# Kernel optimization log

Hardware: AMD Instinct MI355X
Metric: run time of the kernel (lower is better)

The kernel has to match this reference:

```python
import jax, jax.numpy as jnp
import numpy as np

WINDOW = 5
MAX_LEVELS = 4
EPS = 1e-6

_SX = (jnp.array([[-1., 0., 1.], [-2., 0., 2.], [-1., 0., 1.]], dtype=jnp.float32) / 8.0).reshape(1, 1, 3, 3)
_SY = jnp.transpose(_SX, (0, 1, 3, 2))
_DN = ('NCHW', 'OIHW', 'NCHW')


def _avg_pool2(x):
    B, C, H, W = x.shape
    return x.reshape(B, C, H // 2, 2, W // 2, 2).mean(axis=(3, 5))


def _warp(img, flow):
    # bilinear grid_sample, align_corners=True, zeros padding; sample at pixel coords grid+flow
    B, C, H, W = img.shape
    ys, xs = jnp.meshgrid(jnp.arange(H, dtype=img.dtype), jnp.arange(W, dtype=img.dtype), indexing='ij')
    x = xs[None] + flow[:, 0]  # [B,H,W]
    y = ys[None] + flow[:, 1]
    x0f, y0f = jnp.floor(x), jnp.floor(y)
    wx, wy = x - x0f, y - y0f
    imf = img.reshape(B, C, H * W)

    def gather(yi, xi):
        valid = (xi >= 0) & (xi <= W - 1) & (yi >= 0) & (yi <= H - 1)
        xi_c = jnp.clip(xi, 0, W - 1).astype(jnp.int32)
        yi_c = jnp.clip(yi, 0, H - 1).astype(jnp.int32)
        flat = (yi_c * W + xi_c).reshape(B, 1, H * W)
        v = jnp.take_along_axis(imf, jnp.broadcast_to(flat, (B, C, H * W)), axis=2).reshape(B, C, H, W)
        return v * valid[:, None].astype(img.dtype)

    out = (gather(y0f, x0f) * ((1 - wx) * (1 - wy))[:, None]
           + gather(y0f, x0f + 1) * (wx * (1 - wy))[:, None]
           + gather(y0f + 1, x0f) * ((1 - wx) * wy)[:, None]
           + gather(y0f + 1, x0f + 1) * (wx * wy)[:, None])
    return out


def _resize_ac(x, Hn, Wn):
    # bilinear resize, align_corners=True (static shapes)
    B, C, H, W = x.shape
    if (H, W) == (Hn, Wn):
        return x
    ys = jnp.linspace(0.0, H - 1, Hn, dtype=x.dtype)
    xs = jnp.linspace(0.0, W - 1, Wn, dtype=x.dtype)
    y0 = jnp.clip(jnp.floor(ys), 0, H - 2).astype(jnp.int32)
    x0 = jnp.clip(jnp.floor(xs), 0, W - 2).astype(jnp.int32)
    wy = (ys - y0)[None, None, :, None]
    wx = (xs - x0)[None, None, None, :]
    rows = x[:, :, y0, :] * (1 - wy) + x[:, :, y0 + 1, :] * wy
    return rows[:, :, :, x0] * (1 - wx) + rows[:, :, :, x0 + 1] * wx


def _lucas_kanade(I1, I2):
    if I1.shape[1] > 1:
        I1 = I1.mean(1, keepdims=True)
        I2 = I2.mean(1, keepdims=True)
    Ix = jax.lax.conv_general_dilated(I1, _SX, (1, 1), [(1, 1), (1, 1)], dimension_numbers=_DN)
    Iy = jax.lax.conv_general_dilated(I1, _SY, (1, 1), [(1, 1), (1, 1)], dimension_numbers=_DN)
    It = I2 - I1
    # stack all 5 structure-tensor products and box-filter them with one grouped conv
    stats = jnp.concatenate([Ix * Ix, Iy * Iy, Ix * Iy, Ix * It, Iy * It], axis=1)  # [B,5,H,W]
    boxk = jnp.ones((5, 1, WINDOW, WINDOW), dtype=I1.dtype)
    p0 = WINDOW // 2
    p1 = WINDOW - p0 - 1
    S = jax.lax.conv_general_dilated(stats, boxk, (1, 1), [(p0, p1), (p0, p1)],
                                     feature_group_count=5, dimension_numbers=_DN)
    Sxx, Syy, Sxy, Sxt, Syt = jnp.split(S, 5, axis=1)
    inv = 1.0 / (Sxx * Syy - Sxy * Sxy + EPS)
    u = (-Syy * Sxt + Sxy * Syt) * inv
    v = (Sxy * Sxt - Sxx * Syt) * inv
    return jnp.concatenate([u, v], axis=1)


def setup_inputs() -> dict:
    key = jax.random.key(0)
    k1, k2 = jax.random.split(key)
    img1 = jax.random.uniform(k1, (8, 3, 512, 512), dtype=jnp.float32)
    img2 = jax.random.uniform(k2, (8, 3, 512, 512), dtype=jnp.float32)
    return {"img1": img1, "img2": img2}


def reference(img1, img2):
    B, C, H, W = img1.shape
    levels = max(1, MAX_LEVELS)
    pyr1, pyr2 = [img1], [img2]
    for _ in range(1, levels):
        pyr1.append(_avg_pool2(pyr1[-1]))
        pyr2.append(_avg_pool2(pyr2[-1]))
    flow = jnp.zeros((B, 2, pyr1[-1].shape[2], pyr1[-1].shape[3]), dtype=img1.dtype)
    for lvl in range(levels - 1, -1, -1):
        I1, I2 = pyr1[lvl], pyr2[lvl]
        if lvl < levels - 1:
            flow = _resize_ac(flow, I1.shape[2], I1.shape[3]) * 2.0
        I2w = _warp(I2, flow)
        flow = flow + _lucas_kanade(I1, I2w)
    if flow.shape[2:] != (H, W):
        fh, fw = flow.shape[2], flow.shape[3]
        flow = _resize_ac(flow, H, W)
        flow = flow * jnp.array([W / fw, H / fh], dtype=flow.dtype).reshape(1, 2, 1, 1)
    return flow
```

## Files before the change

### kernel.cpp

```cpp
#include <hip/hip_runtime.h>

#define NB 8

typedef float f2 __attribute__((ext_vector_type(2)));


__device__ __forceinline__ void gray_item(
    int i, const float* __restrict__ img1, const float* __restrict__ img2,
    float* __restrict__ g0a, float* __restrict__ g0b,
    float* __restrict__ g1a, float* __restrict__ g1b) {
    const int W = 512, HW = 512 * 512, Wq = 256, HWq = 256 * 256;
    int qx = i % Wq;
    int qy = (i / Wq) % Wq;
    int b = i / HWq;
    size_t base = (size_t)b * 3 * HW + (size_t)(2 * qy) * W + 2 * qx;
    const float third = 1.0f / 3.0f;

    f2 a0c0 = __builtin_nontemporal_load((const f2*)(img1 + base));
    f2 a1c0 = __builtin_nontemporal_load((const f2*)(img1 + base + W));
    f2 a0c1 = __builtin_nontemporal_load((const f2*)(img1 + base + HW));
    f2 a1c1 = __builtin_nontemporal_load((const f2*)(img1 + base + HW + W));
    f2 a0c2 = __builtin_nontemporal_load((const f2*)(img1 + base + 2 * HW));
    f2 a1c2 = __builtin_nontemporal_load((const f2*)(img1 + base + 2 * HW + W));
    float p00 = (a0c0.x + a0c1.x + a0c2.x) * third;
    float p01 = (a0c0.y + a0c1.y + a0c2.y) * third;
    float p10 = (a1c0.x + a1c1.x + a1c2.x) * third;
    float p11 = (a1c0.y + a1c1.y + a1c2.y) * third;
    size_t gbase = (size_t)b * HW + (size_t)(2 * qy) * W + 2 * qx;
    *(f2*)(g0a + gbase) = (f2){p00, p01};
    *(f2*)(g0a + gbase + W) = (f2){p10, p11};
    g1a[(size_t)b * HWq + qy * Wq + qx] = (p00 + p01 + p10 + p11) * 0.25f;

    f2 b0c0 = __builtin_nontemporal_load((const f2*)(img2 + base));
    f2 b1c0 = __builtin_nontemporal_load((const f2*)(img2 + base + W));
    f2 b0c1 = __builtin_nontemporal_load((const f2*)(img2 + base + HW));
    f2 b1c1 = __builtin_nontemporal_load((const f2*)(img2 + base + HW + W));
    f2 b0c2 = __builtin_nontemporal_load((const f2*)(img2 + base + 2 * HW));
    f2 b1c2 = __builtin_nontemporal_load((const f2*)(img2 + base + 2 * HW + W));
    float q00 = (b0c0.x + b0c1.x + b0c2.x) * third;
    float q01 = (b0c0.y + b0c1.y + b0c2.y) * third;
    float q10 = (b1c0.x + b1c1.x + b1c2.x) * third;
    float q11 = (b1c0.y + b1c1.y + b1c2.y) * third;
    *(f2*)(g0b + gbase) = (f2){q00, q01};
    *(f2*)(g0b + gbase + W) = (f2){q10, q11};
    g1b[(size_t)b * HWq + qy * Wq + qx] = (q00 + q01 + q10 + q11) * 0.25f;
}

__device__ __forceinline__ void down2_item(
    int i, const float* __restrict__ l1a, const float* __restrict__ l1b,
    float* __restrict__ l2a, float* __restrict__ l2b,
    float* __restrict__ l3a, float* __restrict__ l3b) {
    const int W3 = 64, W2 = 128, W1 = 256;
    int x3 = i % W3;
    int y3 = (i / W3) % W3;
    int b = (i / (W3 * W3)) % NB;
    int j = i / (NB * W3 * W3);
    const float* l1 = (j ? l1b : l1a) + (size_t)b * W1 * W1;
    float* l2 = (j ? l2b : l2a) + (size_t)b * W2 * W2;
    float* l3 = (j ? l3b : l3a) + (size_t)b * W3 * W3;
    float4 r0 = *(const float4*)(l1 + (size_t)(4 * y3 + 0) * W1 + 4 * x3);
    float4 r1 = *(const float4*)(l1 + (size_t)(4 * y3 + 1) * W1 + 4 * x3);
    float4 r2 = *(const float4*)(l1 + (size_t)(4 * y3 + 2) * W1 + 4 * x3);
    float4 r3 = *(const float4*)(l1 + (size_t)(4 * y3 + 3) * W1 + 4 * x3);
    float a00 = (r0.x + r0.y + r1.x + r1.y) * 0.25f;
    float a01 = (r0.z + r0.w + r1.z + r1.w) * 0.25f;
    float a10 = (r2.x + r2.y + r3.x + r3.y) * 0.25f;
    float a11 = (r2.z + r2.w + r3.z + r3.w) * 0.25f;
    *(f2*)(l2 + (size_t)(2 * y3) * W2 + 2 * x3) = (f2){a00, a01};
    *(f2*)(l2 + (size_t)(2 * y3 + 1) * W2 + 2 * x3) = (f2){a10, a11};
    l3[y3 * W3 + x3] = (a00 + a01 + a10 + a11) * 0.25f;
}

template <int MODE, int H, int W, int TH>
__device__ __forceinline__ void lk_strip(
    int b, int tix, const float* __restrict__ g1, const float* __restrict__ g2,
    const float* __restrict__ fin, float* __restrict__ fout) {
    constexpr int XT = (W + 57) / 58;
    constexpr int NR = TH + 4;
    constexpr int Hs = H / 2, Ws = W / 2;
    constexpr float scale = (float)(Hs - 1) / (float)(H - 1);

    const int lane = threadIdx.x & 63;
    const int xt = tix % XT, yt = tix / XT;
    const int x = xt * 58 - 3 + lane;
    const bool xin = (x >= 0) && (x < W);

    const float* G1 = g1 + (size_t)b * H * W;
    const float* G2 = g2 + (size_t)b * H * W;
    float* FO = fout + (size_t)b * 2 * H * W;

    const int p0 = yt * TH - 2;

    auto issue1 = [&](int yy) -> float {
        return (xin && yy >= 0 && yy < H) ? G1[yy * W + x] : 0.0f;
    };
    auto dands = [&](float gv, float& d, float& s) {
        float gl = __shfl_up(gv, 1);
        float gr = __shfl_down(gv, 1);
        d = gr - gl;
        s = gl + 2.0f * gv + gr;
    };
    auto hs5 = [&](float v) {
        float a = __shfl_down(v, 1);
        float c = __shfl_down(v, 2);
        float t = v + a + c;
        return __shfl_up(t, 2) + a + c;
    };

    float g[NR + 2];
#pragma unroll
    for (int j = 0; j < NR + 2; ++j) g[j] = issue1(p0 - 1 + j);

    float i2d[MODE ? 1 : NR];
    if (!MODE) {
#pragma unroll
        for (int i = 0; i < NR; ++i) {
            int yc = p0 + i;
            i2d[i] = (xin && yc >= 0 && yc < H) ? G2[yc * W + x] : 0.0f;
        }
    }

    float su[MODE ? NR : 1], sv[MODE ? NR : 1];
    float w00[MODE ? NR : 1], w01[MODE ? NR : 1], w10[MODE ? NR : 1], w11[MODE ? NR : 1];
    if (MODE) {
        const float* FU = fin + (size_t)b * 2 * Hs * Ws;
        const float* FV = FU + Hs * Ws;
        float sx = (float)x * scale;
        int cx0 = min(max((int)sx, 0), Ws - 2);
        float wxf = sx - (float)cx0;
        int y0cur = min(max((int)((float)p0 * scale), 0), Hs - 2);
        const float* pu = FU + y0cur * Ws + cx0;
        const float* pv = FV + y0cur * Ws + cx0;
        float u00 = pu[0], u01 = pu[1], u10 = pu[Ws], u11 = pu[Ws + 1];
        float v00 = pv[0], v01 = pv[1], v10 = pv[Ws], v11 = pv[Ws + 1];
#pragma unroll
        for (int i = 0; i < NR; ++i) {
            int yc = p0 + i;
            int y0i = min(max((int)((float)yc * scale), 0), Hs - 2);
            if (y0i != y0cur) {
                u00 = u10; u01 = u11; v00 = v10; v01 = v11;
                const float* qu = FU + (y0i + 1) * Ws + cx0;
                const float* qv = FV + (y0i + 1) * Ws + cx0;
                u10 = qu[0]; u11 = qu[1];
                v10 = qv[0]; v11 = qv[1];
                y0cur = y0i;
            }
            float wyf = (float)yc * scale - (float)y0cur;
            float ut = u00 + (u10 - u00) * wyf;
            float ub = u01 + (u11 - u01) * wyf;
            float vt = v00 + (v10 - v00) * wyf;
            float vb = v01 + (v11 - v01) * wyf;
            su[i] = 2.0f * (ut + (ub - ut) * wxf);
            sv[i] = 2.0f * (vt + (vb - vt) * wxf);
            float xx = (float)x + su[i], yy2 = (float)yc + sv[i];
            int xi = (int)floorf(xx), yi = (int)floorf(yy2);
            int xa = min(max(xi, 0), W - 1), xb = min(max(xi + 1, 0), W - 1);
            int ya = min(max(yi, 0), H - 1), yb = min(max(yi + 1, 0), H - 1);
            w00[i] = G2[ya * W + xa];
            w01[i] = G2[ya * W + xb];
            w10[i] = G2[yb * W + xa];
            w11[i] = G2[yb * W + xb];
        }
    }

    float hxx[5], hyy[5], hxy[5], hxt[5], hyt[5];
#pragma unroll
    for (int k = 0; k < 5; ++k) { hxx[k] = hyy[k] = hxy[k] = hxt[k] = hyt[k] = 0.0f; }

    float dm, d0, sm, s0, dp, sp;
    dands(g[0], dm, sm);
    dands(g[1], d0, s0);

#pragma unroll
    for (int i = 0; i < NR; ++i) {
        const int yc = p0 + i;
        dands(g[i + 2], dp, sp);
        float Ix = (dm + 2.0f * d0 + dp) * 0.125f;
        float Iy = (sp - sm) * 0.125f;

        float I2w;
        if (MODE) {
            float xx = (float)x + su[i], yy2 = (float)yc + sv[i];
            float x0f = floorf(xx), y0f = floorf(yy2);
            float wx = xx - x0f, wy = yy2 - y0f;
            int xi = (int)x0f, yi = (int)y0f;
            float mx0 = (xi >= 0 && xi < W) ? 1.0f : 0.0f;
            float mx1 = (xi >= -1 && xi < W - 1) ? 1.0f : 0.0f;
            float my0 = (yi >= 0 && yi < H) ? 1.0f : 0.0f;
            float my1 = (yi >= -1 && yi < H - 1) ? 1.0f : 0.0f;
            I2w = w00[i] * ((1.0f - wx) * (1.0f - wy) * mx0 * my0)
                + w01[i] * (wx * (1.0f - wy) * mx1 * my0)
                + w10[i] * ((1.0f - wx) * wy * mx0 * my1)
                + w11[i] * (wx * wy * mx1 * my1);
        } else {
            I2w = i2d[i];
        }
        float It = I2w - g[i + 1];
        float vm = (xin && yc >= 0 && yc < H) ? 1.0f : 0.0f;
        Ix *= vm; Iy *= vm; It *= vm;

        const int k = i % 5;
        hxx[k] = Ix * Ix;
        hyy[k] = Iy * Iy;
        hxy[k] = Ix * Iy;
        hxt[k] = Ix * It;
        hyt[k] = Iy * It;

        if (i >= 4) {
            float vxx = hxx[0] + hxx[1] + hxx[2] + hxx[3] + hxx[4];
            float vyy = hyy[0] + hyy[1] + hyy[2] + hyy[3] + hyy[4];
            float vxy = hxy[0] + hxy[1] + hxy[2] + hxy[3] + hxy[4];
            float vxt = hxt[0] + hxt[1] + hxt[2] + hxt[3] + hxt[4];
            float vyt = hyt[0] + hyt[1] + hyt[2] + hyt[3] + hyt[4];
            float Sxx = hs5(vxx);
            float Syy = hs5(vyy);
            float Sxy = hs5(vxy);
            float Sxt = hs5(vxt);
            float Syt = hs5(vyt);
            float inv = 1.0f / (Sxx * Syy - Sxy * Sxy + 1e-6f);
            float du = (-Syy * Sxt + Sxy * Syt) * inv;
            float dv = (Sxy * Sxt - Sxx * Syt) * inv;
            int yo = yc - 2;
            if (lane >= 3 && lane <= 60 && x < W) {
                float ou = du, ov = dv;
                if (MODE) { ou += su[i - 2]; ov += sv[i - 2]; }
                FO[yo * W + x] = ou;
                FO[H * W + yo * W + x] = ov;
            }
        }
        dm = d0; d0 = dp;
        sm = s0; s0 = sp;
    }
}


__global__ void gray_pool_kernel(const float* __restrict__ img1, const float* __restrict__ img2,
                                 float* __restrict__ g0a, float* __restrict__ g0b,
                                 float* __restrict__ g1a, float* __restrict__ g1b) {
    int i = blockIdx.x * blockDim.x + threadIdx.x;
    if (i >= NB * 256 * 256) return;
    gray_item(i, img1, img2, g0a, g0b, g1a, g1b);
}

__global__ void down2_kernel(const float* __restrict__ l1a, const float* __restrict__ l1b,
                             float* __restrict__ l2a, float* __restrict__ l2b,
                             float* __restrict__ l3a, float* __restrict__ l3b) {
    int i = blockIdx.x * blockDim.x + threadIdx.x;
    if (i >= 2 * NB * 64 * 64) return;
    down2_item(i, l1a, l1b, l2a, l2b, l3a, l3b);
}

template <int MODE, int H, int W, int TH>
__global__ __launch_bounds__(256, 4) void lk_roll(
    const float* __restrict__ g1, const float* __restrict__ g2,
    const float* __restrict__ fin, float* __restrict__ fout) {
    constexpr int XT = (W + 57) / 58;
    constexpr int TILES = XT * (H / TH);
    const int wid = threadIdx.x >> 6;
    const int b = blockIdx.x % NB;
    const int tix = (blockIdx.x / NB) * 4 + wid;
    if (tix >= TILES) return;
    lk_strip<MODE, H, W, TH>(b, tix, g1, g2, fin, fout);
}

extern "C" void kernel_launch(void* const* d_in, const int* in_sizes, int n_in,
                              void* d_out, int out_size, void* d_ws, size_t ws_size,
                              hipStream_t stream) {
    const float* img1 = (const float*)d_in[0];
    const float* img2 = (const float*)d_in[1];
    float* out = (float*)d_out;
    float* ws = (float*)d_ws;

    constexpr size_t HW0 = 512 * 512, HW1 = 256 * 256, HW2 = 128 * 128, HW3 = 64 * 64;
    constexpr size_t TOT = NB * (HW0 + HW1 + HW2 + HW3);
    float* p1 = ws;
    float* p2 = ws + TOT;
    float* f64 = p2 + TOT;
    float* f128 = f64 + NB * 2 * HW3;
    float* f256 = f128 + NB * 2 * HW2;
    float* p1_0 = p1, * p1_1 = p1 + NB * HW0, * p1_2 = p1_1 + NB * HW1, * p1_3 = p1_2 + NB * HW2;
    float* p2_0 = p2, * p2_1 = p2 + NB * HW0, * p2_2 = p2_1 + NB * HW1, * p2_3 = p2_2 + NB * HW2;

    {
        int n = NB * 256 * 256;
        gray_pool_kernel<<<(n + 255) / 256, 256, 0, stream>>>(img1, img2, p1_0, p2_0, p1_1, p2_1);
    }
    {
        int n = 2 * NB * 64 * 64;
        down2_kernel<<<(n + 255) / 256, 256, 0, stream>>>(p1_1, p2_1, p1_2, p2_2, p1_3, p2_3);
    }
    {
        constexpr int tiles = 2 * 64;
        lk_roll<0, 64, 64, 1><<<NB * ((tiles + 3) / 4), 256, 0, stream>>>(p1_3, p2_3, nullptr, f64);
    }
    {
        constexpr int tiles = 3 * 128;
        lk_roll<1, 128, 128, 1><<<NB * ((tiles + 3) / 4), 256, 0, stream>>>(p1_2, p2_2, f64, f128);
    }
    {
        constexpr int tiles = 5 * 128;
        lk_roll<1, 256, 256, 2><<<NB * ((tiles + 3) / 4), 256, 0, stream>>>(p1_1, p2_1, f128, f256);
    }
    {
        constexpr int tiles = 9 * 128;
        lk_roll<1, 512, 512, 4><<<NB * ((tiles + 3) / 4), 256, 0, stream>>>(p1_0, p2_0, f256, out);
    }
}
```

Before: 64.14 us.

## Fuse grayscale and full pyramid construction into one tiled kernel

Replaces the separate gray/pool and down2 kernels with a single kernel. Each block handles a 16x16 tile of level 1 and builds levels 2 and 3 from shared memory, which removes one launch and the global re-read of level 1. It adds two block barriers with mostly idle threads in the later stages, and block-to-tile mapping changes coalescing (16-wide rows). Separately, the flow upsampling loop now reloads four neighbours per row instead of carrying rows over, which simplifies control flow at the cost of extra cached loads.

```diff
diff --git a/kernel.cpp b/kernel.cpp
--- a/kernel.cpp
+++ b/kernel.cpp
@@ -4,16 +4,24 @@
 
 typedef float f2 __attribute__((ext_vector_type(2)));
 
-
-__device__ __forceinline__ void gray_item(
-    int i, const float* __restrict__ img1, const float* __restrict__ img2,
+__global__ __launch_bounds__(256) void gray_pyr_kernel(
+    const float* __restrict__ img1, const float* __restrict__ img2,
     float* __restrict__ g0a, float* __restrict__ g0b,
-    float* __restrict__ g1a, float* __restrict__ g1b) {
-    const int W = 512, HW = 512 * 512, Wq = 256, HWq = 256 * 256;
-    int qx = i % Wq;
-    int qy = (i / Wq) % Wq;
-    int b = i / HWq;
-    size_t base = (size_t)b * 3 * HW + (size_t)(2 * qy) * W + 2 * qx;
+    float* __restrict__ g1a, float* __restrict__ g1b,
+    float* __restrict__ g2a, float* __restrict__ g2b,
+    float* __restrict__ g3a, float* __restrict__ g3b) {
+    const int W = 512, HW = 512 * 512;
+    __shared__ float sL1a[16][17], sL1b[16][17];
+    __shared__ float sL2a[8][9], sL2b[8][9];
+
+    int blk = blockIdx.x;
+    int b = blk % NB;
+    int t = blk / NB;
+    int ty = t / 16, tx = t % 16;
+    int lx = threadIdx.x % 16, ly = threadIdx.x / 16;
+    int y1 = ty * 16 + ly, x1 = tx * 16 + lx;
+
+    size_t base = (size_t)b * 3 * HW + (size_t)(2 * y1) * W + 2 * x1;
     const float third = 1.0f / 3.0f;
 
     f2 a0c0 = __builtin_nontemporal_load((const f2*)(img1 + base));
@@ -26,10 +34,12 @@
     float p01 = (a0c0.y + a0c1.y + a0c2.y) * third;
     float p10 = (a1c0.x + a1c1.x + a1c2.x) * third;
     float p11 = (a1c0.y + a1c1.y + a1c2.y) * third;
-    size_t gbase = (size_t)b * HW + (size_t)(2 * qy) * W + 2 * qx;
+    size_t gbase = (size_t)b * HW + (size_t)(2 * y1) * W + 2 * x1;
     *(f2*)(g0a + gbase) = (f2){p00, p01};
     *(f2*)(g0a + gbase + W) = (f2){p10, p11};
-    g1a[(size_t)b * HWq + qy * Wq + qx] = (p00 + p01 + p10 + p11) * 0.25f;
+    float pa = (p00 + p01 + p10 + p11) * 0.25f;
+    g1a[(size_t)b * 256 * 256 + y1 * 256 + x1] = pa;
+    sL1a[ly][lx] = pa;
 
     f2 b0c0 = __builtin_nontemporal_load((const f2*)(img2 + base));
     f2 b1c0 = __builtin_nontemporal_load((const f2*)(img2 + base + W));
@@ -43,32 +53,33 @@
     float q11 = (b1c0.y + b1c1.y + b1c2.y) * third;
     *(f2*)(g0b + gbase) = (f2){q00, q01};
     *(f2*)(g0b + gbase + W) = (f2){q10, q11};
-    g1b[(size_t)b * HWq + qy * Wq + qx] = (q00 + q01 + q10 + q11) * 0.25f;
-}
-
-__device__ __forceinline__ void down2_item(
-    int i, const float* __restrict__ l1a, const float* __restrict__ l1b,
-    float* __restrict__ l2a, float* __restrict__ l2b,
-    float* __restrict__ l3a, float* __restrict__ l3b) {
-    const int W3 = 64, W2 = 128, W1 = 256;
-    int x3 = i % W3;
-    int y3 = (i / W3) % W3;
-    int b = (i / (W3 * W3)) % NB;
-    int j = i / (NB * W3 * W3);
-    const float* l1 = (j ? l1b : l1a) + (size_t)b * W1 * W1;
-    float* l2 = (j ? l2b : l2a) + (size_t)b * W2 * W2;
-    float* l3 = (j ? l3b : l3a) + (size_t)b * W3 * W3;
-    float4 r0 = *(const float4*)(l1 + (size_t)(4 * y3 + 0) * W1 + 4 * x3);
-    float4 r1 = *(const float4*)(l1 + (size_t)(4 * y3 + 1) * W1 + 4 * x3);
-    float4 r2 = *(const float4*)(l1 + (size_t)(4 * y3 + 2) * W1 + 4 * x3);
-    float4 r3 = *(const float4*)(l1 + (size_t)(4 * y3 + 3) * W1 + 4 * x3);
-    float a00 = (r0.x + r0.y + r1.x + r1.y) * 0.25f;
-    float a01 = (r0.z + r0.w + r1.z + r1.w) * 0.25f;
-    float a10 = (r2.x + r2.y + r3.x + r3.y) * 0.25f;
-    float a11 = (r2.z + r2.w + r3.z + r3.w) * 0.25f;
-    *(f2*)(l2 + (size_t)(2 * y3) * W2 + 2 * x3) = (f2){a00, a01};
-    *(f2*)(l2 + (size_t)(2 * y3 + 1) * W2 + 2 * x3) = (f2){a10, a11};
-    l3[y3 * W3 + x3] = (a00 + a01 + a10 + a11) * 0.25f;
+    float pb = (q00 + q01 + q10 + q11) * 0.25f;
+    g1b[(size_t)b * 256 * 256 + y1 * 256 + x1] = pb;
+    sL1b[ly][lx] = pb;
+    __syncthreads();
+
+    if (threadIdx.x < 64) {
+        int y2 = threadIdx.x / 8, x2 = threadIdx.x % 8;
+        float va = (sL1a[2 * y2][2 * x2] + sL1a[2 * y2][2 * x2 + 1]
+                  + sL1a[2 * y2 + 1][2 * x2] + sL1a[2 * y2 + 1][2 * x2 + 1]) * 0.25f;
+        float vb = (sL1b[2 * y2][2 * x2] + sL1b[2 * y2][2 * x2 + 1]
+                  + sL1b[2 * y2 + 1][2 * x2] + sL1b[2 * y2 + 1][2 * x2 + 1]) * 0.25f;
+        g2a[(size_t)b * 128 * 128 + (ty * 8 + y2) * 128 + tx * 8 + x2] = va;
+        g2b[(size_t)b * 128 * 128 + (ty * 8 + y2) * 128 + tx * 8 + x2] = vb;
+        sL2a[y2][x2] = va;
+        sL2b[y2][x2] = vb;
+    }
+    __syncthreads();
+
+    if (threadIdx.x < 16) {
+        int y3 = threadIdx.x / 4, x3 = threadIdx.x % 4;
+        float va = (sL2a[2 * y3][2 * x3] + sL2a[2 * y3][2 * x3 + 1]
+                  + sL2a[2 * y3 + 1][2 * x3] + sL2a[2 * y3 + 1][2 * x3 + 1]) * 0.25f;
+        float vb = (sL2b[2 * y3][2 * x3] + sL2b[2 * y3][2 * x3 + 1]
+                  + sL2b[2 * y3 + 1][2 * x3] + sL2b[2 * y3 + 1][2 * x3 + 1]) * 0.25f;
+        g3a[(size_t)b * 64 * 64 + (ty * 4 + y3) * 64 + tx * 4 + x3] = va;
+        g3b[(size_t)b * 64 * 64 + (ty * 4 + y3) * 64 + tx * 4 + x3] = vb;
+    }
 }
 
 template <int MODE, int H, int W, int TH>
@@ -128,24 +139,15 @@
         float sx = (float)x * scale;
         int cx0 = min(max((int)sx, 0), Ws - 2);
         float wxf = sx - (float)cx0;
-        int y0cur = min(max((int)((float)p0 * scale), 0), Hs - 2);
-        const float* pu = FU + y0cur * Ws + cx0;
-        const float* pv = FV + y0cur * Ws + cx0;
-        float u00 = pu[0], u01 = pu[1], u10 = pu[Ws], u11 = pu[Ws + 1];
-        float v00 = pv[0], v01 = pv[1], v10 = pv[Ws], v11 = pv[Ws + 1];
 #pragma unroll
         for (int i = 0; i < NR; ++i) {
             int yc = p0 + i;
             int y0i = min(max((int)((float)yc * scale), 0), Hs - 2);
-            if (y0i != y0cur) {
-                u00 = u10; u01 = u11; v00 = v10; v01 = v11;
-                const float* qu = FU + (y0i + 1) * Ws + cx0;
-                const float* qv = FV + (y0i + 1) * Ws + cx0;
-                u10 = qu[0]; u11 = qu[1];
-                v10 = qv[0]; v11 = qv[1];
-                y0cur = y0i;
-            }
-            float wyf = (float)yc * scale - (float)y0cur;
+            float wyf = (float)yc * scale - (float)y0i;
+            const float* pu = FU + y0i * Ws + cx0;
+            const float* pv = FV + y0i * Ws + cx0;
+            float u00 = pu[0], u01 = pu[1], u10 = pu[Ws], u11 = pu[Ws + 1];
+            float v00 = pv[0], v01 = pv[1], v10 = pv[Ws], v11 = pv[Ws + 1];
             float ut = u00 + (u10 - u00) * wyf;
             float ub = u01 + (u11 - u01) * wyf;
             float vt = v00 + (v10 - v00) * wyf;
@@ -233,23 +235,6 @@
     }
 }
 
-
-__global__ void gray_pool_kernel(const float* __restrict__ img1, const float* __restrict__ img2,
-                                 float* __restrict__ g0a, float* __restrict__ g0b,
-                                 float* __restrict__ g1a, float* __restrict__ g1b) {
-    int i = blockIdx.x * blockDim.x + threadIdx.x;
-    if (i >= NB * 256 * 256) return;
-    gray_item(i, img1, img2, g0a, g0b, g1a, g1b);
-}
-
-__global__ void down2_kernel(const float* __restrict__ l1a, const float* __restrict__ l1b,
-                             float* __restrict__ l2a, float* __restrict__ l2b,
-                             float* __restrict__ l3a, float* __restrict__ l3b) {
-    int i = blockIdx.x * blockDim.x + threadIdx.x;
-    if (i >= 2 * NB * 64 * 64) return;
-    down2_item(i, l1a, l1b, l2a, l2b, l3a, l3b);
-}
-
 template <int MODE, int H, int W, int TH>
 __global__ __launch_bounds__(256, 4) void lk_roll(
     const float* __restrict__ g1, const float* __restrict__ g2,
@@ -281,14 +266,9 @@
     float* p1_0 = p1, * p1_1 = p1 + NB * HW0, * p1_2 = p1_1 + NB * HW1, * p1_3 = p1_2 + NB * HW2;
     float* p2_0 = p2, * p2_1 = p2 + NB * HW0, * p2_2 = p2_1 + NB * HW1, * p2_3 = p2_2 + NB * HW2;
 
-    {
-        int n = NB * 256 * 256;
-        gray_pool_kernel<<<(n + 255) / 256, 256, 0, stream>>>(img1, img2, p1_0, p2_0, p1_1, p2_1);
-    }
-    {
-        int n = 2 * NB * 64 * 64;
-        down2_kernel<<<(n + 255) / 256, 256, 0, stream>>>(p1_1, p2_1, p1_2, p2_2, p1_3, p2_3);
-    }
+    gray_pyr_kernel<<<NB * 256, 256, 0, stream>>>(
+        img1, img2, p1_0, p2_0, p1_1, p2_1, p1_2, p2_2, p1_3, p2_3);
+
     {
         constexpr int tiles = 2 * 64;
         lk_roll<0, 64, 64, 1><<<NB * ((tiles + 3) / 4), 256, 0, stream>>>(p1_3, p2_3, nullptr, f64);
```

Result: slower. 69.44 us (+8.3%).
